# Optimization experiments

Hardware: AMD Instinct MI355X
Metric: run time of the kernel (lower is better)

The kernel has to match this reference:

```python
import jax, jax.numpy as jnp
import numpy as np

D_MODEL = 1024
NUM_HEADS = 16
HEAD_DIM = D_MODEL // NUM_HEADS
NUM_KERNELS = 21


def tisa_bias(amp, off, sharp, seq_len):
    # amp/off/sharp: (H, K). Returns (H, L, L) translation-invariant bias.
    # Evaluate on the 2L-1 distinct relative distances, then gather (Toeplitz).
    d = jnp.arange(-(seq_len - 1), seq_len, dtype=amp.dtype)  # (2L-1,)
    # (H, K, 2L-1) -> sum over kernels -> (H, 2L-1)
    scores = jnp.sum(
        amp[:, :, None]
        * jnp.exp(-jnp.abs(sharp)[:, :, None] * (d[None, None, :] - off[:, :, None]) ** 2),
        axis=1,
    )
    i = jnp.arange(seq_len)
    rel_idx = i[None, :] - i[:, None] + (seq_len - 1)  # (L, L) in [0, 2L-2]
    return scores[:, rel_idx]  # (H, L, L)


def setup_inputs() -> dict:
    key = jax.random.key(0)
    ks = jax.random.split(key, 9)
    B, L = 4, 1024
    s = 0.02
    return {
        "x_q": jax.random.normal(ks[0], (B, L, D_MODEL), dtype=jnp.float32),
        "x_kv": jax.random.normal(ks[1], (B, L, D_MODEL), dtype=jnp.float32),
        "Wq": jax.random.normal(ks[2], (D_MODEL, D_MODEL), dtype=jnp.float32) * s,
        "Wm": jax.random.normal(ks[3], (D_MODEL, 2 * D_MODEL), dtype=jnp.float32) * s,
        "Wg": jax.random.normal(ks[4], (D_MODEL, 2 * D_MODEL), dtype=jnp.float32) * s,
        "bg": jnp.zeros((2 * D_MODEL,), dtype=jnp.float32),
        "tisa_amp": jax.random.normal(ks[5], (NUM_HEADS, NUM_KERNELS), dtype=jnp.float32) * 0.1,
        "tisa_off": jax.random.uniform(ks[6], (NUM_HEADS, NUM_KERNELS), dtype=jnp.float32, minval=-512.0, maxval=512.0),
        "tisa_sharp": jax.random.uniform(ks[7], (NUM_HEADS, NUM_KERNELS), dtype=jnp.float32, minval=1e-4, maxval=0.05),
    }


def reference(x_q, x_kv, Wq, Wm, Wg, bg, tisa_amp, tisa_off, tisa_sharp):
    B, Lq, _ = x_q.shape
    Lkv = x_kv.shape[1]
    H, Dh = NUM_HEADS, HEAD_DIM

    q = (x_q @ Wq).reshape(B, Lq, H, Dh).transpose(0, 2, 1, 3)        # (B,H,Lq,Dh)
    mem = (x_kv @ Wm)                                                 # (B,Lkv,2D)
    k = mem[..., :D_MODEL].reshape(B, Lkv, H, Dh).transpose(0, 2, 1, 3)
    v = mem[..., D_MODEL:].reshape(B, Lkv, H, Dh).transpose(0, 2, 1, 3)

    scale = 1.0 / jnp.sqrt(jnp.asarray(Dh, dtype=q.dtype))
    scores = jnp.einsum("bhqd,bhkd->bhqk", q, k) * scale              # (B,H,Lq,Lkv)
    scores = scores + tisa_bias(tisa_amp, tisa_off, tisa_sharp, Lkv)[None]
    weights = jax.nn.softmax(scores, axis=-1)

    attn = jnp.einsum("bhqk,bhkd->bhqd", weights, v)                  # (B,H,Lq,Dh)
    attn = attn.transpose(0, 2, 1, 3).reshape(B, Lq, D_MODEL)

    g = attn @ Wg + bg                                                # (B,Lq,2D)
    a, b = g[..., :D_MODEL], g[..., D_MODEL:]
    return a * jax.nn.sigmoid(b)
```

## Files before the change

### kernel.cpp

```cpp
#include <hip/hip_runtime.h>
#include <cstdint>
#include <cstddef>

typedef __attribute__((ext_vector_type(8))) short bf16x8;
typedef __attribute__((ext_vector_type(4))) float f32x4;

#define LOG2E 1.44269504f

__device__ __forceinline__ unsigned short f2bf(float x) {
  unsigned int u = __float_as_uint(x);
  u += 0x7FFFu + ((u >> 16) & 1u);
  return (unsigned short)(u >> 16);
}

__device__ __forceinline__ void gload_lds16(const void* g, void* l) {
  __builtin_amdgcn_global_load_lds(
      (const __attribute__((address_space(1))) unsigned int*)g,
      (__attribute__((address_space(3))) unsigned int*)l, 16, 0, 0);
}


__global__ void cast_f32_bf16(const float4* __restrict__ src,
                              ushort4* __restrict__ dst, int n4) {
  int i = blockIdx.x * 256 + threadIdx.x;
  if (i < n4) {
    float4 v = src[i];
    ushort4 o;
    o.x = f2bf(v.x); o.y = f2bf(v.y); o.z = f2bf(v.z); o.w = f2bf(v.w);
    dst[i] = o;
  }
}

__global__ void transpose_cast(const float* __restrict__ src,
                               unsigned short* __restrict__ dst,
                               int K, int N) {
  __shared__ float tile[32][33];
  int nb = blockIdx.x * 32, kb = blockIdx.y * 32;
  int tx = threadIdx.x & 31, ty = threadIdx.x >> 5;
#pragma unroll
  for (int r = ty; r < 32; r += 8)
    tile[r][tx] = src[(size_t)(kb + r) * N + nb + tx];
  __syncthreads();
#pragma unroll
  for (int r = ty; r < 32; r += 8)
    dst[(size_t)(nb + r) * K + kb + tx] = f2bf(tile[tx][r]);
}

__global__ void bias_tab_kernel(const float* __restrict__ amp,
                                const float* __restrict__ off,
                                const float* __restrict__ sharp,
                                float* __restrict__ tab) {
  int h = blockIdx.x;
  for (int idx = threadIdx.x; idx < 2047; idx += 256) {
    float d = (float)(idx - 1023);
    float acc = 0.f;
#pragma unroll
    for (int k = 0; k < 21; ++k) {
      float dd = d - off[h * 21 + k];
      acc += amp[h * 21 + k] * __expf(-fabsf(sharp[h * 21 + k]) * dd * dd);
    }
    tab[h * 2047 + idx] = acc * LOG2E;
  }
}


__global__ __launch_bounds__(256)
void qkv_gemm(const unsigned short* __restrict__ Xq,
              const unsigned short* __restrict__ Xkv,
              const unsigned short* __restrict__ WqT,
              const unsigned short* __restrict__ WmT,
              unsigned short* __restrict__ qbuf,
              unsigned short* __restrict__ kbuf,
              unsigned short* __restrict__ vtbuf) {
  __shared__ unsigned short sA[128 * 32];
  __shared__ unsigned short sB[128 * 32];
  const int bx = blockIdx.x;
  const bool isQ = bx < 8;
  const int ntile = (isQ ? bx : bx - 8) << 7;
  const unsigned short* A = isQ ? Xq : Xkv;
  const unsigned short* B = (isQ ? WqT : WmT) + (size_t)ntile * 1024;
  const int t = threadIdx.x, lane = t & 63, w = t >> 6;
  const int wm = (w >> 1) << 6, wn = (w & 1) << 6;
  const int mtile = blockIdx.y << 7;
  const int c = lane & 15, g = lane >> 4;
  const int srow = t >> 2, scol = (t & 3) << 3;
  const unsigned short* aP = A + (size_t)(mtile + srow) * 1024 + scol;
  const unsigned short* bP = B + (size_t)srow * 1024 + scol;
  unsigned short* sAd = &sA[srow * 32 + scol];
  unsigned short* sBd = &sB[srow * 32 + scol];
  f32x4 acc[4][4] = {};

  for (int kt = 0; kt < 1024; kt += 32) {
    gload_lds16(aP + kt, sAd);
    gload_lds16(aP + (size_t)64 * 1024 + kt, sAd + 64 * 32);
    gload_lds16(bP + kt, sBd);
    gload_lds16(bP + (size_t)64 * 1024 + kt, sBd + 64 * 32);
    __syncthreads();
    bf16x8 af[4], bfr[4];
#pragma unroll
    for (int i = 0; i < 4; ++i) {
      af[i]  = *(const bf16x8*)&sA[(wm + i * 16 + c) * 32 + g * 8];
      bfr[i] = *(const bf16x8*)&sB[(wn + i * 16 + c) * 32 + g * 8];
    }
#pragma unroll
    for (int i = 0; i < 4; ++i)
#pragma unroll
      for (int j = 0; j < 4; ++j)
        acc[i][j] = __builtin_amdgcn_mfma_f32_16x16x32_bf16(af[i], bfr[j], acc[i][j], 0, 0, 0);
    __syncthreads();
  }

  const int row0 = mtile + wm + (g << 2);
  const int col0 = ntile + wn + c;
  if (isQ) {
#pragma unroll
    for (int i = 0; i < 4; ++i)
#pragma unroll
      for (int j = 0; j < 4; ++j) {
        int r = row0 + i * 16, cl = col0 + j * 16;
#pragma unroll
        for (int ri = 0; ri < 4; ++ri)
          qbuf[(size_t)(r + ri) * 1024 + cl] = f2bf(acc[i][j][ri] * (0.125f * LOG2E));
      }
  } else {
#pragma unroll
    for (int i = 0; i < 4; ++i)
#pragma unroll
      for (int j = 0; j < 4; ++j) {
        int r = row0 + i * 16, cl = col0 + j * 16;
        if (cl < 1024) {
#pragma unroll
          for (int ri = 0; ri < 4; ++ri)
            kbuf[(size_t)(r + ri) * 1024 + cl] = f2bf(acc[i][j][ri]);
        } else {
          int d = cl - 1024;
          int hh = d >> 6, dh = d & 63;
          int bb = r >> 10, ll = r & 1023;
          ushort4 pk;
          pk.x = f2bf(acc[i][j][0]);
          pk.y = f2bf(acc[i][j][1]);
          pk.z = f2bf(acc[i][j][2]);
          pk.w = f2bf(acc[i][j][3]);
          *(ushort4*)&vtbuf[((size_t)((bb * 16 + hh) * 64 + dh) << 10) + ll] = pk;
        }
      }
  }
}


__global__ __launch_bounds__(512)
void attn_kernel(const unsigned short* __restrict__ qbuf,
                 const unsigned short* __restrict__ kbuf,
                 const unsigned short* __restrict__ vtbuf,
                 const float* __restrict__ biasTab,
                 unsigned short* __restrict__ attnb) {
  const int qt = blockIdx.x, h = blockIdx.y, b = blockIdx.z;
  __shared__ unsigned short sQ[128 * 64];
  __shared__ unsigned short sK[2][64 * 64];
  __shared__ unsigned short sV[2][64 * 64];
  __shared__ unsigned short sP[8][16 * 64];
  const int t = threadIdx.x, lane = t & 63, w = t >> 6;
  const int c = lane & 15, g = lane >> 4;

  const int r = t >> 3, pc = t & 7, ch = pc ^ (r & 7);

  const unsigned short* qsrc = qbuf + (size_t)(b * 1024 + qt * 128) * 1024 + h * 64;
  const unsigned short* ksrc = kbuf + (size_t)(b * 1024) * 1024 + h * 64;
  const unsigned short* vsrc = vtbuf + (size_t)((b * 16 + h) * 64) * 1024;

  gload_lds16(qsrc + (size_t)r * 1024 + ch * 8, &sQ[t * 8]);
  gload_lds16(qsrc + (size_t)(r + 64) * 1024 + ch * 8, &sQ[4096 + t * 8]);
  gload_lds16(ksrc + (size_t)r * 1024 + ch * 8, &sK[0][t * 8]);
  gload_lds16(vsrc + (size_t)r * 1024 + ch * 8, &sV[0][t * 8]);
  __syncthreads();

  const int qrow = w * 16 + c;
  const int qx = (qrow & 7) * 8;
  bf16x8 aq0 = *(const bf16x8*)&sQ[qrow * 64 + ((g * 8) ^ qx)];
  bf16x8 aq1 = *(const bf16x8*)&sQ[qrow * 64 + (((g + 4) * 8) ^ qx)];

  f32x4 o[4] = {};
  float lsum[4] = {0.f, 0.f, 0.f, 0.f};
  const int qrow0 = qt * 128 + w * 16 + g * 4;
  const float* bbase = biasTab + h * 2047 + 1023 + c - qrow0;

  for (int kv = 0; kv < 16; ++kv) {
    const int cur = kv & 1;
    if (kv + 1 < 16) {
      gload_lds16(ksrc + (size_t)((kv + 1) * 64 + r) * 1024 + ch * 8, &sK[1 - cur][t * 8]);
      gload_lds16(vsrc + (size_t)r * 1024 + (kv + 1) * 64 + ch * 8, &sV[1 - cur][t * 8]);
    }

    f32x4 s[4];
#pragma unroll
    for (int nf = 0; nf < 4; ++nf) {
      int krow = nf * 16 + c;
      int kx = (krow & 7) * 8;
      bf16x8 b0 = *(const bf16x8*)&sK[cur][krow * 64 + ((g * 8) ^ kx)];
      bf16x8 b1 = *(const bf16x8*)&sK[cur][krow * 64 + (((g + 4) * 8) ^ kx)];
      f32x4 z = {};
      z = __builtin_amdgcn_mfma_f32_16x16x32_bf16(aq0, b0, z, 0, 0, 0);
      z = __builtin_amdgcn_mfma_f32_16x16x32_bf16(aq1, b1, z, 0, 0, 0);
      s[nf] = z;
    }

    const float* bk = bbase + kv * 64;
#pragma unroll
    for (int nf = 0; nf < 4; ++nf)
#pragma unroll
      for (int ri = 0; ri < 4; ++ri) {
        float e = exp2f(s[nf][ri] + bk[nf * 16 - ri]);
        lsum[ri] += e;
        int prow = g * 4 + ri;
        sP[w][prow * 64 + (((2 * nf + (c >> 3)) ^ (prow & 7)) * 8) + (c & 7)] = f2bf(e);
      }

    int px = (c & 7) * 8;
    bf16x8 ap0 = *(const bf16x8*)&sP[w][c * 64 + ((g * 8) ^ px)];
    bf16x8 ap1 = *(const bf16x8*)&sP[w][c * 64 + (((g + 4) * 8) ^ px)];
#pragma unroll
    for (int nf = 0; nf < 4; ++nf) {
      int vrow = nf * 16 + c;
      int vx = (vrow & 7) * 8;
      bf16x8 b0 = *(const bf16x8*)&sV[cur][vrow * 64 + ((g * 8) ^ vx)];
      bf16x8 b1 = *(const bf16x8*)&sV[cur][vrow * 64 + (((g + 4) * 8) ^ vx)];
      o[nf] = __builtin_amdgcn_mfma_f32_16x16x32_bf16(ap0, b0, o[nf], 0, 0, 0);
      o[nf] = __builtin_amdgcn_mfma_f32_16x16x32_bf16(ap1, b1, o[nf], 0, 0, 0);
    }
    __syncthreads();
  }

#pragma unroll
  for (int off = 1; off < 16; off <<= 1)
#pragma unroll
    for (int ri = 0; ri < 4; ++ri)
      lsum[ri] += __shfl_xor(lsum[ri], off, 64);
  float rinv[4];
#pragma unroll
  for (int ri = 0; ri < 4; ++ri) rinv[ri] = 1.0f / lsum[ri];

  unsigned short* obase = attnb + (size_t)(b * 1024 + qt * 128 + w * 16 + g * 4) * 1024 + h * 64;
#pragma unroll
  for (int nf = 0; nf < 4; ++nf)
#pragma unroll
    for (int ri = 0; ri < 4; ++ri)
      obase[(size_t)ri * 1024 + nf * 16 + c] = f2bf(o[nf][ri] * rinv[ri]);
}


__global__ __launch_bounds__(256)
void out_gemm(const unsigned short* __restrict__ A,
              const unsigned short* __restrict__ WgT,
              const float* __restrict__ bg,
              float* __restrict__ out) {
  __shared__ unsigned short sA[128 * 32];
  __shared__ unsigned short sB[128 * 32];
  const int nb = blockIdx.x;
  const int mtile = blockIdx.y << 7;
  const int t = threadIdx.x, lane = t & 63, w = t >> 6;
  const int c = lane & 15, g = lane >> 4;
  const int srow = t >> 2, scol = (t & 3) << 3;
  const unsigned short* aP = A + (size_t)(mtile + srow) * 1024 + scol;
  const unsigned short* bP0 = WgT + (size_t)(nb * 64 + srow) * 1024 + scol;
  const unsigned short* bP1 = WgT + (size_t)(1024 + nb * 64 + srow) * 1024 + scol;
  unsigned short* sAd = &sA[srow * 32 + scol];
  unsigned short* sBd = &sB[srow * 32 + scol];
  f32x4 acc[2][8] = {};

  for (int kt = 0; kt < 1024; kt += 32) {
    gload_lds16(aP + kt, sAd);
    gload_lds16(aP + (size_t)64 * 1024 + kt, sAd + 64 * 32);
    gload_lds16(bP0 + kt, sBd);
    gload_lds16(bP1 + kt, sBd + 64 * 32);
    __syncthreads();
    bf16x8 af[2], bfr[8];
#pragma unroll
    for (int i = 0; i < 2; ++i)
      af[i] = *(const bf16x8*)&sA[(w * 32 + i * 16 + c) * 32 + g * 8];
#pragma unroll
    for (int j = 0; j < 8; ++j)
      bfr[j] = *(const bf16x8*)&sB[(j * 16 + c) * 32 + g * 8];
#pragma unroll
    for (int i = 0; i < 2; ++i)
#pragma unroll
      for (int j = 0; j < 8; ++j)
        acc[i][j] = __builtin_amdgcn_mfma_f32_16x16x32_bf16(af[i], bfr[j], acc[i][j], 0, 0, 0);
    __syncthreads();
  }

#pragma unroll
  for (int i = 0; i < 2; ++i) {
    int row0 = mtile + w * 32 + i * 16 + (g << 2);
#pragma unroll
    for (int jj = 0; jj < 4; ++jj) {
      int col = nb * 64 + jj * 16 + c;
      float ba = bg[col];
      float bb = bg[1024 + col];
#pragma unroll
      for (int ri = 0; ri < 4; ++ri) {
        float av = acc[i][jj][ri] + ba;
        float bv = acc[i][jj + 4][ri] + bb;
        out[(size_t)(row0 + ri) * 1024 + col] = av / (1.f + exp2f(-LOG2E * bv));
      }
    }
  }
}


extern "C" void kernel_launch(void* const* d_in, const int* in_sizes, int n_in,
                              void* d_out, int out_size, void* d_ws, size_t ws_size,
                              hipStream_t stream) {
  const float* x_q   = (const float*)d_in[0];
  const float* x_kv  = (const float*)d_in[1];
  const float* Wq    = (const float*)d_in[2];
  const float* Wm    = (const float*)d_in[3];
  const float* Wg    = (const float*)d_in[4];
  const float* bg    = (const float*)d_in[5];
  const float* amp   = (const float*)d_in[6];
  const float* off   = (const float*)d_in[7];
  const float* sharp = (const float*)d_in[8];
  float* out = (float*)d_out;

  char* ws = (char*)d_ws;
  size_t o = 0;
  auto alloc = [&](size_t bytes) {
    char* p = ws + o;
    o += (bytes + 255) & ~(size_t)255;
    return p;
  };
  unsigned short* bXq   = (unsigned short*)alloc(4096ull * 1024 * 2);
  unsigned short* bXkv  = (unsigned short*)alloc(4096ull * 1024 * 2);
  unsigned short* bWqT  = (unsigned short*)alloc(1024ull * 1024 * 2);
  unsigned short* bWmT  = (unsigned short*)alloc(2048ull * 1024 * 2);
  unsigned short* bWgT  = (unsigned short*)alloc(2048ull * 1024 * 2);
  float*          biasT = (float*)alloc(16ull * 2047 * 4);
  unsigned short* qbuf  = (unsigned short*)alloc(4096ull * 1024 * 2);
  unsigned short* kbuf  = (unsigned short*)alloc(4096ull * 1024 * 2);
  unsigned short* vtbuf = (unsigned short*)alloc(4096ull * 1024 * 2);
  unsigned short* attnb = (unsigned short*)alloc(4096ull * 1024 * 2);
  if (ws_size < o) return;

  cast_f32_bf16<<<4096, 256, 0, stream>>>((const float4*)x_q,  (ushort4*)bXq,  1024 * 1024);
  cast_f32_bf16<<<4096, 256, 0, stream>>>((const float4*)x_kv, (ushort4*)bXkv, 1024 * 1024);
  transpose_cast<<<dim3(32, 32), 256, 0, stream>>>(Wq, bWqT, 1024, 1024);
  transpose_cast<<<dim3(64, 32), 256, 0, stream>>>(Wm, bWmT, 1024, 2048);
  transpose_cast<<<dim3(64, 32), 256, 0, stream>>>(Wg, bWgT, 1024, 2048);
  bias_tab_kernel<<<16, 256, 0, stream>>>(amp, off, sharp, biasT);

  qkv_gemm<<<dim3(24, 32), 256, 0, stream>>>(bXq, bXkv, bWqT, bWmT, qbuf, kbuf, vtbuf);
  attn_kernel<<<dim3(8, 16, 4), 512, 0, stream>>>(qbuf, kbuf, vtbuf, biasT, attnb);
  out_gemm<<<dim3(16, 32), 256, 0, stream>>>(attnb, bWgT, bg, out);
}
```

Before: 237.8 us.

## Double-buffer LDS tiles in the GEMMs and merge the preprocessing launches

Both the QKV and output GEMMs now keep two LDS tile buffers and issue the global-to-LDS loads for the next K slice before computing on the current one. This is meant to overlap memory latency with MFMA work, at the cost of twice the shared memory per block, which may reduce occupancy. Separately, the two input cast kernels are merged into one launch, and the three weight transpose-casts into one launch using the z grid dimension, to cut launch overhead. In the merged transpose launch, blocks beyond the narrower Wq matrix exit early.

```diff
diff --git a/kernel.cpp b/kernel.cpp
--- a/kernel.cpp
+++ b/kernel.cpp
@@ -20,22 +20,34 @@
 }
 
 
-__global__ void cast_f32_bf16(const float4* __restrict__ src,
-                              ushort4* __restrict__ dst, int n4) {
+__global__ void cast2_f32_bf16(const float4* __restrict__ xq,
+                               const float4* __restrict__ xkv,
+                               ushort4* __restrict__ dq,
+                               ushort4* __restrict__ dkv) {
   int i = blockIdx.x * 256 + threadIdx.x;
-  if (i < n4) {
-    float4 v = src[i];
-    ushort4 o;
-    o.x = f2bf(v.x); o.y = f2bf(v.y); o.z = f2bf(v.z); o.w = f2bf(v.w);
-    dst[i] = o;
-  }
-}
-
-__global__ void transpose_cast(const float* __restrict__ src,
-                               unsigned short* __restrict__ dst,
-                               int K, int N) {
+  const float4* s;
+  ushort4* d;
+  if (i < (1 << 20)) { s = xq; d = dq; }
+  else { s = xkv + ((1 << 20) * -1); d = dkv - (1 << 20); }
+  float4 v = s[i];
+  ushort4 o;
+  o.x = f2bf(v.x); o.y = f2bf(v.y); o.z = f2bf(v.z); o.w = f2bf(v.w);
+  d[i] = o;
+}
+
+__global__ void transpose_cast3(const float* __restrict__ Wq,
+                                const float* __restrict__ Wm,
+                                const float* __restrict__ Wg,
+                                unsigned short* __restrict__ dWq,
+                                unsigned short* __restrict__ dWm,
+                                unsigned short* __restrict__ dWg) {
   __shared__ float tile[32][33];
+  int z = blockIdx.z;
+  const float* src = z == 0 ? Wq : (z == 1 ? Wm : Wg);
+  unsigned short* dst = z == 0 ? dWq : (z == 1 ? dWm : dWg);
+  int N = z == 0 ? 1024 : 2048;
   int nb = blockIdx.x * 32, kb = blockIdx.y * 32;
+  if (nb >= N) return;
   int tx = threadIdx.x & 31, ty = threadIdx.x >> 5;
 #pragma unroll
   for (int r = ty; r < 32; r += 8)
@@ -43,7 +55,7 @@
   __syncthreads();
 #pragma unroll
   for (int r = ty; r < 32; r += 8)
-    dst[(size_t)(nb + r) * K + kb + tx] = f2bf(tile[tx][r]);
+    dst[(size_t)(nb + r) * 1024 + kb + tx] = f2bf(tile[tx][r]);
 }
 
 __global__ void bias_tab_kernel(const float* __restrict__ amp,
@@ -72,8 +84,8 @@
               unsigned short* __restrict__ qbuf,
               unsigned short* __restrict__ kbuf,
               unsigned short* __restrict__ vtbuf) {
-  __shared__ unsigned short sA[128 * 32];
-  __shared__ unsigned short sB[128 * 32];
+  __shared__ unsigned short sA[2][128 * 32];
+  __shared__ unsigned short sB[2][128 * 32];
   const int bx = blockIdx.x;
   const bool isQ = bx < 8;
   const int ntile = (isQ ? bx : bx - 8) << 7;
@@ -86,21 +98,29 @@
   const int srow = t >> 2, scol = (t & 3) << 3;
   const unsigned short* aP = A + (size_t)(mtile + srow) * 1024 + scol;
   const unsigned short* bP = B + (size_t)srow * 1024 + scol;
-  unsigned short* sAd = &sA[srow * 32 + scol];
-  unsigned short* sBd = &sB[srow * 32 + scol];
+  const int lo = srow * 32 + scol;
+
+  gload_lds16(aP, &sA[0][lo]);
+  gload_lds16(aP + 64 * 1024, &sA[0][lo + 64 * 32]);
+  gload_lds16(bP, &sB[0][lo]);
+  gload_lds16(bP + 64 * 1024, &sB[0][lo + 64 * 32]);
+  __syncthreads();
+
   f32x4 acc[4][4] = {};
-
-  for (int kt = 0; kt < 1024; kt += 32) {
-    gload_lds16(aP + kt, sAd);
-    gload_lds16(aP + (size_t)64 * 1024 + kt, sAd + 64 * 32);
-    gload_lds16(bP + kt, sBd);
-    gload_lds16(bP + (size_t)64 * 1024 + kt, sBd + 64 * 32);
-    __syncthreads();
+  for (int kt = 0; kt < 32; ++kt) {
+    const int cur = kt & 1;
+    if (kt + 1 < 32) {
+      const int ko = (kt + 1) * 32;
+      gload_lds16(aP + ko, &sA[1 - cur][lo]);
+      gload_lds16(aP + 64 * 1024 + ko, &sA[1 - cur][lo + 64 * 32]);
+      gload_lds16(bP + ko, &sB[1 - cur][lo]);
+      gload_lds16(bP + 64 * 1024 + ko, &sB[1 - cur][lo + 64 * 32]);
+    }
     bf16x8 af[4], bfr[4];
 #pragma unroll
     for (int i = 0; i < 4; ++i) {
-      af[i]  = *(const bf16x8*)&sA[(wm + i * 16 + c) * 32 + g * 8];
-      bfr[i] = *(const bf16x8*)&sB[(wn + i * 16 + c) * 32 + g * 8];
+      af[i]  = *(const bf16x8*)&sA[cur][(wm + i * 16 + c) * 32 + g * 8];
+      bfr[i] = *(const bf16x8*)&sB[cur][(wn + i * 16 + c) * 32 + g * 8];
     }
 #pragma unroll
     for (int i = 0; i < 4; ++i)
@@ -253,8 +273,8 @@
               const unsigned short* __restrict__ WgT,
               const float* __restrict__ bg,
               float* __restrict__ out) {
-  __shared__ unsigned short sA[128 * 32];
-  __shared__ unsigned short sB[128 * 32];
+  __shared__ unsigned short sA[2][128 * 32];
+  __shared__ unsigned short sB[2][128 * 32];
   const int nb = blockIdx.x;
   const int mtile = blockIdx.y << 7;
   const int t = threadIdx.x, lane = t & 63, w = t >> 6;
@@ -263,23 +283,31 @@
   const unsigned short* aP = A + (size_t)(mtile + srow) * 1024 + scol;
   const unsigned short* bP0 = WgT + (size_t)(nb * 64 + srow) * 1024 + scol;
   const unsigned short* bP1 = WgT + (size_t)(1024 + nb * 64 + srow) * 1024 + scol;
-  unsigned short* sAd = &sA[srow * 32 + scol];
-  unsigned short* sBd = &sB[srow * 32 + scol];
+  const int lo = srow * 32 + scol;
+
+  gload_lds16(aP, &sA[0][lo]);
+  gload_lds16(aP + 64 * 1024, &sA[0][lo + 64 * 32]);
+  gload_lds16(bP0, &sB[0][lo]);
+  gload_lds16(bP1, &sB[0][lo + 64 * 32]);
+  __syncthreads();
+
   f32x4 acc[2][8] = {};
-
-  for (int kt = 0; kt < 1024; kt += 32) {
-    gload_lds16(aP + kt, sAd);
-    gload_lds16(aP + (size_t)64 * 1024 + kt, sAd + 64 * 32);
-    gload_lds16(bP0 + kt, sBd);
-    gload_lds16(bP1 + kt, sBd + 64 * 32);
-    __syncthreads();
+  for (int kt = 0; kt < 32; ++kt) {
+    const int cur = kt & 1;
+    if (kt + 1 < 32) {
+      const int ko = (kt + 1) * 32;
+      gload_lds16(aP + ko, &sA[1 - cur][lo]);
+      gload_lds16(aP + 64 * 1024 + ko, &sA[1 - cur][lo + 64 * 32]);
+      gload_lds16(bP0 + ko, &sB[1 - cur][lo]);
+      gload_lds16(bP1 + ko, &sB[1 - cur][lo + 64 * 32]);
+    }
     bf16x8 af[2], bfr[8];
 #pragma unroll
     for (int i = 0; i < 2; ++i)
-      af[i] = *(const bf16x8*)&sA[(w * 32 + i * 16 + c) * 32 + g * 8];
+      af[i] = *(const bf16x8*)&sA[cur][(w * 32 + i * 16 + c) * 32 + g * 8];
 #pragma unroll
     for (int j = 0; j < 8; ++j)
-      bfr[j] = *(const bf16x8*)&sB[(j * 16 + c) * 32 + g * 8];
+      bfr[j] = *(const bf16x8*)&sB[cur][(j * 16 + c) * 32 + g * 8];
 #pragma unroll
     for (int i = 0; i < 2; ++i)
 #pragma unroll
@@ -340,11 +368,9 @@
   unsigned short* attnb = (unsigned short*)alloc(4096ull * 1024 * 2);
   if (ws_size < o) return;
 
-  cast_f32_bf16<<<4096, 256, 0, stream>>>((const float4*)x_q,  (ushort4*)bXq,  1024 * 1024);
-  cast_f32_bf16<<<4096, 256, 0, stream>>>((const float4*)x_kv, (ushort4*)bXkv, 1024 * 1024);
-  transpose_cast<<<dim3(32, 32), 256, 0, stream>>>(Wq, bWqT, 1024, 1024);
-  transpose_cast<<<dim3(64, 32), 256, 0, stream>>>(Wm, bWmT, 1024, 2048);
-  transpose_cast<<<dim3(64, 32), 256, 0, stream>>>(Wg, bWgT, 1024, 2048);
+  cast2_f32_bf16<<<8192, 256, 0, stream>>>((const float4*)x_q, (const float4*)x_kv,
+                                           (ushort4*)bXq, (ushort4*)bXkv);
+  transpose_cast3<<<dim3(64, 32, 3), 256, 0, stream>>>(Wq, Wm, Wg, bWqT, bWmT, bWgT);
   bias_tab_kernel<<<16, 256, 0, stream>>>(amp, off, sharp, biasT);
 
   qkv_gemm<<<dim3(24, 32), 256, 0, stream>>>(bXq, bXkv, bWqT, bWmT, qbuf, kbuf, vtbuf);
```

New measurement: 222.0 us. 6.6% less time.
